# Kernel tuning notes

Measured on AMD Instinct MI355X. Metric: run time of the kernel, lower is better.

The kernel has to match this reference:

```python
import jax, jax.numpy as jnp
import numpy as np


def setup_inputs() -> dict:
    key = jax.random.key(0)
    ks = jax.random.split(key, 7)
    B, T, E, D = 4, 4096, 1024, 64
    s = 1.0 / np.sqrt(E)
    return {
        "x": jax.random.normal(ks[0], (B, T, E), dtype=jnp.float32),
        "Wq": jax.random.normal(ks[1], (E, D), dtype=jnp.float32) * s,
        "bq": jnp.zeros((D,), dtype=jnp.float32),
        "Wk": jax.random.normal(ks[2], (E, D), dtype=jnp.float32) * s,
        "bk": jnp.zeros((D,), dtype=jnp.float32),
        "Wv": jax.random.normal(ks[3], (E, D), dtype=jnp.float32) * s,
        "bv": jnp.zeros((D,), dtype=jnp.float32),
    }


def reference(x, Wq, bq, Wk, bk, Wv, bv):
    # Linear projections (torch Linear with W stored as [in, out])
    q = x @ Wq + bq  # [B, T, D]
    k = x @ Wk + bk  # [B, T, D]
    v = x @ Wv + bv  # [B, T, D]
    d_k = q.shape[-1]
    scale = 1.0 / jnp.sqrt(jnp.asarray(d_k, dtype=q.dtype))
    scores = jnp.einsum("btd,bsd->bts", q, k) * scale  # [B, T, T]
    att = jax.nn.softmax(scores, axis=-1)
    # dropout p=0.0 -> identity (eval-mode reference)
    out = jnp.einsum("bts,bsd->btd", att, v)  # [B, T, D]
    return out
```

## Files before the change

kernel.cpp:

```cpp
#include <hip/hip_runtime.h>

typedef __attribute__((ext_vector_type(4))) float f32x4;
typedef __attribute__((ext_vector_type(16))) float f32x16;
typedef __attribute__((ext_vector_type(8))) short s16x8;
typedef __attribute__((ext_vector_type(4))) short s16x4;
typedef __attribute__((ext_vector_type(4))) unsigned u32x4;

#define BATCH 4
#define SEQ 4096
#define EMB 1024
#define HD 64
#define QSCALE (0.125f * 1.44269504088896f)
#define M0 32.0f

static __device__ __forceinline__ unsigned short f2bf(float f) {
  union { float f; unsigned int u; } a;
  a.f = f;
  unsigned int u = a.u;
  u += 0x7FFFu + ((u >> 16) & 1u);
  return (unsigned short)(u >> 16);
}

static __device__ __forceinline__ float fexp2(float x) {
  return __builtin_amdgcn_exp2f(x);
}
static __device__ __forceinline__ void swap32u(unsigned& a, unsigned& b) {
  asm("s_nop 0\n\tv_permlane32_swap_b32 %0, %1\n\ts_nop 0" : "+v"(a), "+v"(b));
}
static __device__ __forceinline__ unsigned cvtpk(float lo, float hi) {
  unsigned r;
  asm("v_cvt_pk_bf16_f32 %0, %1, %2" : "=v"(r) : "v"(lo), "v"(hi));
  return r;
}

#define GLL16(g, l)                                                        \
  __builtin_amdgcn_global_load_lds(                                        \
      (const __attribute__((address_space(1))) unsigned int*)(g),          \
      (__attribute__((address_space(3))) unsigned int*)(l), 16, 0, 0)

__global__ __launch_bounds__(256) void k_wt(const float* __restrict__ Wq,
                                            const float* __restrict__ Wk,
                                            const float* __restrict__ Wv,
                                            unsigned short* __restrict__ wt) {
  __shared__ float lds[64][65];
  int tid = threadIdx.x;
  int which = blockIdx.x >> 4;
  int kt = blockIdx.x & 15;
  const float* W = (which == 0) ? Wq : ((which == 1) ? Wk : Wv);
#pragma unroll
  for (int i = 0; i < 4; ++i) {
    int idx = i * 256 + tid;
    int row = idx >> 4, c4 = idx & 15;
    float4 v = *(const float4*)(W + (size_t)(kt * 64 + row) * 64 + c4 * 4);
    lds[row][c4 * 4 + 0] = v.x;
    lds[row][c4 * 4 + 1] = v.y;
    lds[row][c4 * 4 + 2] = v.z;
    lds[row][c4 * 4 + 3] = v.w;
  }
  __syncthreads();
#pragma unroll
  for (int i = 0; i < 2; ++i) {
    int c = i * 256 + tid;
    int cfl = c >> 7, kk = (c >> 6) & 1, l = c & 63;
    int lg = l >> 4, lc = l & 15;
    s16x8 v;
#pragma unroll
    for (int j = 0; j < 8; ++j) v[j] = (short)f2bf(lds[kk * 32 + lg * 8 + j][cfl * 16 + lc]);
    size_t off = ((((size_t)kt * 12 + (which * 4 + cfl)) * 2 + kk) * 64 + l) * 8;
    *(s16x8*)(wt + off) = v;
  }
}

__global__ __launch_bounds__(256, 2) void k_proj(const float* __restrict__ x,
                                                 const unsigned short* __restrict__ wt,
                                                 const float* __restrict__ bq,
                                                 const float* __restrict__ bk,
                                                 const float* __restrict__ bv,
                                                 unsigned short* __restrict__ qws,
                                                 unsigned short* __restrict__ kws,
                                                 unsigned short* __restrict__ vws) {
  __shared__ char xb[4][8192];
  int tid = threadIdx.x;
  int w = tid >> 6, ln = tid & 63;
  int lg = ln >> 4, lc = ln & 15;
  int m0 = blockIdx.x * 32;

  f32x4 acc[2][3];
#pragma unroll
  for (int s = 0; s < 2; ++s)
#pragma unroll
    for (int c = 0; c < 3; ++c) acc[s][c] = (f32x4){0.f, 0.f, 0.f, 0.f};

  s16x8 bA[3][2], bB[3][2];

  int srow = w * 8 + (ln >> 4);
  int schunk0 = ln & 15;
#define GLLI(kt_, bi_)                                                        \
  _Pragma("unroll") for (int p = 0; p < 2; ++p) {                             \
    int r = srow + p * 4;                                                     \
    const char* src = (const char*)x + (size_t)(m0 + r) * 4096 + (kt_)*256 +  \
                      ((schunk0 ^ (r & 7)) << 4);                             \
    GLL16(src, &xb[bi_][w * 2048 + p * 1024]);                                \
  }
#define BLD(dst_, kt_)                                                        \
  _Pragma("unroll") for (int c = 0; c < 3; ++c)                               \
      _Pragma("unroll") for (int kk = 0; kk < 2; ++kk)                        \
          dst_[c][kk] = *(const s16x8*)(wt + ((size_t)((kt_)*12 + w * 3 + c) * 2 + kk) * 512 + ln * 8);

#define ITER(T_, bcur_, bnext_, NW_)                                          \
  {                                                                           \
    if ((T_) + 1 < 16) BLD(bnext_, (T_) + 1);                                 \
    if ((T_) + 3 < 16) GLLI((T_) + 3, ((T_) + 3) & 3);                        \
    asm volatile("s_waitcnt vmcnt(" #NW_ ")" ::: "memory");                   \
    __builtin_amdgcn_s_barrier();                                             \
    __builtin_amdgcn_sched_barrier(0);                                        \
    s16x8 a[2][2];                                                            \
    _Pragma("unroll") for (int s = 0; s < 2; ++s)                             \
        _Pragma("unroll") for (int kk = 0; kk < 2; ++kk) {                    \
      int g0 = kk * 8 + lg * 2;                                               \
      f32x4 c0 = *(const f32x4*)(&xb[(T_) & 3][(s * 16 + lc) * 256 + ((g0 ^ (lc & 7)) << 4)]); \
      f32x4 c1 = *(const f32x4*)(&xb[(T_) & 3][(s * 16 + lc) * 256 + (((g0 + 1) ^ (lc & 7)) << 4)]); \
      union { u32x4 u; s16x8 v; } cv;                                         \
      cv.u = (u32x4){cvtpk(c0[0], c0[1]), cvtpk(c0[2], c0[3]),                \
                     cvtpk(c1[0], c1[1]), cvtpk(c1[2], c1[3])};               \
      a[s][kk] = cv.v;                                                        \
    }                                                                         \
    __builtin_amdgcn_s_setprio(1);                                            \
    _Pragma("unroll") for (int s = 0; s < 2; ++s)                             \
        _Pragma("unroll") for (int c = 0; c < 3; ++c)                         \
            _Pragma("unroll") for (int kk = 0; kk < 2; ++kk)                  \
                acc[s][c] = __builtin_amdgcn_mfma_f32_16x16x32_bf16(          \
                    a[s][kk], bcur_[c][kk], acc[s][c], 0, 0, 0);              \
    __builtin_amdgcn_s_setprio(0);                                            \
    __builtin_amdgcn_s_barrier();                                             \
  }

  GLLI(0, 0);
  GLLI(1, 1);
  GLLI(2, 2);
  BLD(bA, 0);
  ITER(0, bA, bB, 18)
  ITER(1, bB, bA, 24)
  ITER(2, bA, bB, 30)
  ITER(3, bB, bA, 24)
  ITER(4, bA, bB, 24)
  ITER(5, bB, bA, 24)
  ITER(6, bA, bB, 24)
  ITER(7, bB, bA, 24)
  ITER(8, bA, bB, 24)
  ITER(9, bB, bA, 24)
  ITER(10, bA, bB, 24)
  ITER(11, bB, bA, 24)
  ITER(12, bA, bB, 24)
  ITER(13, bB, bA, 22)
  ITER(14, bA, bB, 20)
  ITER(15, bB, bA, 12)
#undef GLLI
#undef BLD
#undef ITER

  unsigned short* ep = (unsigned short*)&xb[0][0];
#pragma unroll
  for (int c = 0; c < 3; ++c) {
    int cf = w * 3 + c;
    int which = cf >> 2;
    int ncol = (cf & 3) * 16 + lc;
    float bias = (which == 0) ? bq[ncol] : ((which == 1) ? bk[ncol] : bv[ncol]);
    if (which < 2) {
#pragma unroll
      for (int s = 0; s < 2; ++s)
#pragma unroll
        for (int r = 0; r < 4; ++r) {
          int trow = s * 16 + lg * 4 + r;
          float val = acc[s][c][r] + bias;
          if (which == 0) val *= QSCALE;
          int o = (ncol >> 4) * 512 + ((ncol >> 3) & 1) * 256 + trow * 8 + (ncol & 7);
          ep[which * 2048 + o] = f2bf(val);
        }
    } else {
#pragma unroll
      for (int s = 0; s < 2; ++s) {
        s16x4 pk;
#pragma unroll
        for (int r = 0; r < 4; ++r) pk[r] = (short)f2bf(acc[s][c][r] + bias);
        int o = s * 1024 + (ncol >> 5) * 512 + (lg >> 1) * 256 + (ncol & 31) * 8 + (lg & 1) * 4;
        *(s16x4*)(ep + 2 * 2048 + o) = pk;
      }
    }
  }
  __syncthreads();
  {
    int b = m0 >> 12, tt = m0 & 4095;
    unsigned short* qdst = qws + (size_t)b * SEQ * 64 + (tt >> 5) * 2048;
    unsigned short* kdst = kws + (size_t)b * SEQ * 64 + (tt >> 5) * 2048;
    unsigned short* vdst = vws + (size_t)b * SEQ * 64 + (tt >> 4) * 1024;
#pragma unroll
    for (int k = 0; k < 3; ++k) {
      int u = k * 256 + tid;
      s16x8 val = *(const s16x8*)(ep + u * 8);
      int which = u >> 8;
      int o = (u & 255) * 8;
      unsigned short* dst = (which == 0) ? qdst : ((which == 1) ? kdst : vdst);
      *(s16x8*)(dst + o) = val;
    }
  }
}

template <int NS, int REP>
__global__ __launch_bounds__(256, 3) void k_attn(const unsigned short* __restrict__ qf_g,
                                                 const unsigned short* __restrict__ kf_g,
                                                 const unsigned short* __restrict__ vf_g,
                                                 float* __restrict__ part,
                                                 float2* __restrict__ ml) {
  __shared__ char kv[3][16384];
  int tid = threadIdx.x;
  int w = tid >> 6, ln = tid & 63;
  int F = blockIdx.x;
  const int nb = 128 * NS;
  int idx = (F & 7) * (nb >> 3) + (F >> 3);
  int split = idx >> 7;
  int rem = idx & 127;
  int b = rem >> 5, q7 = rem & 31;
  const int TPS = 64 / NS;
  int t0 = split * TPS;

  const unsigned short* qb = qf_g + (size_t)b * SEQ * 64;
  const char* kbytes = (const char*)(kf_g + (size_t)b * SEQ * 64);
  const char* vbytes = (const char*)(vf_g + (size_t)b * SEQ * 64);

  int qrow = q7 * 128 + w * 32;

  s16x8 qf[4];
#pragma unroll
  for (int db = 0; db < 4; ++db)
    qf[db] = *(const s16x8*)(qb + (size_t)(((q7 * 4 + w) * 4 + db) * 512 + ln * 8));

  s16x8 onef;
#pragma unroll
  for (int j = 0; j < 8; ++j) onef[j] = (short)0x3F80;

  f32x16 o_[2], l_acc;

#define STAGE(t_, bi_)                                                        \
  _Pragma("unroll") for (int i = 0; i < 4; ++i) {                             \
    int cc = w * 4 + i;                                                       \
    const char* src = (cc < 8 ? kbytes + (size_t)(t_)*8192 + cc * 1024        \
                              : vbytes + (size_t)(t_)*8192 + (cc - 8) * 1024) \
                      + ln * 16;                                              \
    GLL16(src, &kv[bi_][cc * 1024]);                                          \
  }

#pragma unroll 1
  for (int rep = 0; rep < REP; ++rep) {
#pragma unroll
    for (int dt = 0; dt < 2; ++dt)
#pragma unroll
      for (int i = 0; i < 16; ++i) o_[dt][i] = 0.f;
#pragma unroll
    for (int i = 0; i < 16; ++i) l_acc[i] = 0.f;

    STAGE(t0, 0)
    STAGE(t0 + 1, 1)
    int bi = 0;
#pragma unroll 1
    for (int it = 0; it < TPS; ++it) {
      int t = t0 + it;
      if (it + 2 < TPS) {
        int nbuf = (bi == 0) ? 2 : bi - 1;
        STAGE(t + 2, nbuf)
        asm volatile("s_waitcnt vmcnt(8)" ::: "memory");
      } else if (it + 1 < TPS) {
        asm volatile("s_waitcnt vmcnt(4)" ::: "memory");
      } else {
        asm volatile("s_waitcnt vmcnt(0)" ::: "memory");
      }
      __builtin_amdgcn_s_barrier();
      __builtin_amdgcn_sched_barrier(0);

      s16x8 kfc[2][4];
#pragma unroll
      for (int kt = 0; kt < 2; ++kt)
#pragma unroll
        for (int db = 0; db < 4; ++db)
          kfc[kt][db] = *(const s16x8*)(&kv[bi][(kt * 4 + db) * 1024 + ln * 16]);

      f32x16 s[2];
      __builtin_amdgcn_s_setprio(1);
#pragma unroll
      for (int kt = 0; kt < 2; ++kt) {
        f32x16 a;
#pragma unroll
        for (int i = 0; i < 16; ++i) a[i] = -M0;
#pragma unroll
        for (int db = 0; db < 4; ++db)
          a = __builtin_amdgcn_mfma_f32_32x32x16_bf16(kfc[kt][db], qf[db], a, 0, 0, 0);
        s[kt] = a;
      }
      __builtin_amdgcn_s_setprio(0);

      s16x8 pf[4];
      {
#pragma unroll
        for (int kt = 0; kt < 2; ++kt)
#pragma unroll
          for (int i = 0; i < 16; ++i) s[kt][i] = fexp2(s[kt][i]);
#pragma unroll
        for (int k4 = 0; k4 < 4; ++k4) {
          int kt = k4 >> 1, mr = 2 * (k4 & 1);
          unsigned a0 = cvtpk(s[kt][mr * 4 + 0], s[kt][mr * 4 + 1]);
          unsigned a1 = cvtpk(s[kt][mr * 4 + 2], s[kt][mr * 4 + 3]);
          unsigned b0 = cvtpk(s[kt][mr * 4 + 4], s[kt][mr * 4 + 5]);
          unsigned b1 = cvtpk(s[kt][mr * 4 + 6], s[kt][mr * 4 + 7]);
          swap32u(a0, b0);
          swap32u(a1, b1);
          union { u32x4 u; s16x8 v16; } cvt;
          cvt.u = (u32x4){a0, a1, b0, b1};
          pf[k4] = cvt.v16;
        }
      }

      __builtin_amdgcn_s_setprio(1);
#pragma unroll
      for (int dt = 0; dt < 2; ++dt)
#pragma unroll
        for (int k4 = 0; k4 < 4; ++k4) {
          s16x8 vfr = *(const s16x8*)(&kv[bi][8192 + (k4 * 2 + dt) * 1024 + ln * 16]);
          o_[dt] = __builtin_amdgcn_mfma_f32_32x32x16_bf16(vfr, pf[k4], o_[dt], 0, 0, 0);
        }
#pragma unroll
      for (int k4 = 0; k4 < 4; ++k4)
        l_acc = __builtin_amdgcn_mfma_f32_32x32x16_bf16(onef, pf[k4], l_acc, 0, 0, 0);
      __builtin_amdgcn_s_setprio(0);
      __builtin_amdgcn_s_barrier();
      bi = (bi == 2) ? 0 : bi + 1;
    }
    if (REP > 1) asm volatile("" : "+v"(o_[0]), "+v"(o_[1]), "+v"(l_acc));
  }
#undef STAGE

  float* pb = part + (size_t)(split * 4 + b) * 64 * SEQ;
  int hi = ln >> 5, lq = ln & 31;
  int tq = qrow + lq;
#pragma unroll
  for (int dt = 0; dt < 2; ++dt)
#pragma unroll
    for (int re = 0; re < 16; ++re) {
      int d = dt * 32 + (re & 3) + 8 * (re >> 2) + 4 * hi;
      pb[(size_t)d * SEQ + tq] = o_[dt][re];
    }
  if (ln < 32)
    ml[(size_t)(split * 4 + b) * SEQ + qrow + ln] = make_float2(M0, l_acc[0]);
}

template <int NS>
__global__ __launch_bounds__(256) void k_red(const float* __restrict__ part,
                                             const float2* __restrict__ ml,
                                             float* __restrict__ out) {
  __shared__ float lds[16][65];
  int tid = threadIdx.x;
  int w = tid >> 6, ln = tid & 63;
  int dq = blockIdx.x & 3;
  int t0 = (blockIdx.x >> 2) * 64;
  int b = t0 >> 12;
  int tt = (t0 & 4095) + ln;

  float2 mls[NS];
#pragma unroll
  for (int s = 0; s < NS; ++s) mls[s] = ml[(size_t)(s * 4 + b) * SEQ + tt];
  float M = mls[0].x;
#pragma unroll
  for (int s = 1; s < NS; ++s) M = fmaxf(M, mls[s].x);
  float Lden = 0.f;
#pragma unroll
  for (int s = 0; s < NS; ++s) Lden += mls[s].y * fexp2(mls[s].x - M);
  float inv = 1.0f / Lden;
  float sc[NS];
#pragma unroll
  for (int s = 0; s < NS; ++s) sc[s] = fexp2(mls[s].x - M) * inv;

  float acc[4] = {0.f, 0.f, 0.f, 0.f};
#pragma unroll
  for (int s = 0; s < NS; ++s) {
    const float* pb = part + ((size_t)(s * 4 + b) * 64 + dq * 16 + w * 4) * SEQ + tt;
#pragma unroll
    for (int i = 0; i < 4; ++i) acc[i] += sc[s] * pb[(size_t)i * SEQ];
  }
#pragma unroll
  for (int i = 0; i < 4; ++i) lds[w * 4 + i][ln] = acc[i];
  __syncthreads();
  {
    int tr = tid >> 2, dc = tid & 3;
    f32x4 o;
#pragma unroll
    for (int j = 0; j < 4; ++j) o[j] = lds[dc * 4 + j][tr];
    *(f32x4*)(out + (size_t)(t0 + tr) * 64 + dq * 16 + dc * 4) = o;
  }
}

extern "C" void kernel_launch(void* const* d_in, const int* in_sizes, int n_in,
                              void* d_out, int out_size, void* d_ws, size_t ws_size,
                              hipStream_t stream) {
  const float* x = (const float*)d_in[0];
  const float* Wq = (const float*)d_in[1];
  const float* bq = (const float*)d_in[2];
  const float* Wk = (const float*)d_in[3];
  const float* bk = (const float*)d_in[4];
  const float* Wv = (const float*)d_in[5];
  const float* bv = (const float*)d_in[6];
  float* out = (float*)d_out;

  char* ws = (char*)d_ws;
  unsigned short* wt = (unsigned short*)(ws);
  unsigned short* qws = (unsigned short*)(ws + 0x80000);
  unsigned short* kws = (unsigned short*)(ws + 0x280000);
  unsigned short* vws = (unsigned short*)(ws + 0x480000);
  const size_t base = 0x680000;
  const size_t perSplit = (size_t)16384 * 64 * 4 + (size_t)16384 * 8;

  k_wt<<<48, 256, 0, stream>>>(Wq, Wk, Wv, wt);
  k_proj<<<512, 256, 0, stream>>>(x, wt, bq, bk, bv, qws, kws, vws);

#define RUN_NS(NSV)                                                           \
  {                                                                           \
    float* partp = (float*)(ws + base);                                       \
    float2* mlp = (float2*)(ws + base + (size_t)NSV * 16384 * 64 * 4);        \
    k_attn<NSV, 1><<<128 * NSV, 256, 0, stream>>>(qws, kws, vws, partp, mlp); \
    k_red<NSV><<<1024, 256, 0, stream>>>(partp, mlp, out);                    \
  }

  if (ws_size >= base + 8 * perSplit) {
    RUN_NS(8)
  } else if (ws_size >= base + 4 * perSplit) {
    RUN_NS(4)
  } else if (ws_size >= base + 2 * perSplit) {
    RUN_NS(2)
  } else {
    RUN_NS(1)
  }
#undef RUN_NS
}
```

Before: 61.60 us.

## Halve KV tile to 32 keys, use 4-buffer ring and drop trailing barrier

Each pipeline stage now loads 32 keys instead of 64, so a stage holds 8 KB of K/V, and the ring grows to four buffers. With four buffers and a prefetch distance of two, the end-of-iteration barrier can go, leaving one barrier per step. Less LDS per block and a higher launch_bounds occupancy hint (5) allow more resident blocks. The cost is twice as many iterations, each with a barrier, waitcnt and a shorter MFMA chain, so there is less work per sync point.

```diff
diff --git a/kernel.cpp b/kernel.cpp
--- a/kernel.cpp
+++ b/kernel.cpp
@@ -207,12 +207,12 @@
 }
 
 template <int NS, int REP>
-__global__ __launch_bounds__(256, 3) void k_attn(const unsigned short* __restrict__ qf_g,
+__global__ __launch_bounds__(256, 5) void k_attn(const unsigned short* __restrict__ qf_g,
                                                  const unsigned short* __restrict__ kf_g,
                                                  const unsigned short* __restrict__ vf_g,
                                                  float* __restrict__ part,
                                                  float2* __restrict__ ml) {
-  __shared__ char kv[3][16384];
+  __shared__ char kv[4][8192];
   int tid = threadIdx.x;
   int w = tid >> 6, ln = tid & 63;
   int F = blockIdx.x;
@@ -221,8 +221,8 @@
   int split = idx >> 7;
   int rem = idx & 127;
   int b = rem >> 5, q7 = rem & 31;
-  const int TPS = 64 / NS;
-  int t0 = split * TPS;
+  const int TPS = 128 / NS;
+  int g0 = split * TPS;
 
   const unsigned short* qb = qf_g + (size_t)b * SEQ * 64;
   const char* kbytes = (const char*)(kf_g + (size_t)b * SEQ * 64);
@@ -241,11 +241,11 @@
 
   f32x16 o_[2], l_acc;
 
-#define STAGE(t_, bi_)                                                        \
-  _Pragma("unroll") for (int i = 0; i < 4; ++i) {                             \
-    int cc = w * 4 + i;                                                       \
-    const char* src = (cc < 8 ? kbytes + (size_t)(t_)*8192 + cc * 1024        \
-                              : vbytes + (size_t)(t_)*8192 + (cc - 8) * 1024) \
+#define STAGE(g_, bi_)                                                        \
+  _Pragma("unroll") for (int i = 0; i < 2; ++i) {                             \
+    int cc = w * 2 + i;                                                       \
+    const char* src = (cc < 4 ? kbytes + (size_t)(g_)*4096 + cc * 1024        \
+                              : vbytes + (size_t)(g_)*4096 + (cc - 4) * 1024) \
                       + ln * 16;                                              \
     GLL16(src, &kv[bi_][cc * 1024]);                                          \
   }
@@ -259,58 +259,52 @@
 #pragma unroll
     for (int i = 0; i < 16; ++i) l_acc[i] = 0.f;
 
-    STAGE(t0, 0)
-    STAGE(t0 + 1, 1)
-    int bi = 0;
+    STAGE(g0, 0)
+    STAGE(g0 + 1, 1)
 #pragma unroll 1
     for (int it = 0; it < TPS; ++it) {
-      int t = t0 + it;
+      int g = g0 + it;
+      int bi = it & 3;
       if (it + 2 < TPS) {
-        int nbuf = (bi == 0) ? 2 : bi - 1;
-        STAGE(t + 2, nbuf)
-        asm volatile("s_waitcnt vmcnt(8)" ::: "memory");
+        STAGE(g + 2, (it + 2) & 3)
+        asm volatile("s_waitcnt vmcnt(4)" ::: "memory");
       } else if (it + 1 < TPS) {
-        asm volatile("s_waitcnt vmcnt(4)" ::: "memory");
+        asm volatile("s_waitcnt vmcnt(2)" ::: "memory");
       } else {
         asm volatile("s_waitcnt vmcnt(0)" ::: "memory");
       }
       __builtin_amdgcn_s_barrier();
       __builtin_amdgcn_sched_barrier(0);
 
-      s16x8 kfc[2][4];
-#pragma unroll
-      for (int kt = 0; kt < 2; ++kt)
+      s16x8 kfc[4];
+#pragma unroll
+      for (int db = 0; db < 4; ++db)
+        kfc[db] = *(const s16x8*)(&kv[bi][db * 1024 + ln * 16]);
+
+      f32x16 s;
+      __builtin_amdgcn_s_setprio(1);
+      {
+        f32x16 a;
+#pragma unroll
+        for (int i = 0; i < 16; ++i) a[i] = -M0;
 #pragma unroll
         for (int db = 0; db < 4; ++db)
-          kfc[kt][db] = *(const s16x8*)(&kv[bi][(kt * 4 + db) * 1024 + ln * 16]);
-
-      f32x16 s[2];
-      __builtin_amdgcn_s_setprio(1);
-#pragma unroll
-      for (int kt = 0; kt < 2; ++kt) {
-        f32x16 a;
-#pragma unroll
-        for (int i = 0; i < 16; ++i) a[i] = -M0;
-#pragma unroll
-        for (int db = 0; db < 4; ++db)
-          a = __builtin_amdgcn_mfma_f32_32x32x16_bf16(kfc[kt][db], qf[db], a, 0, 0, 0);
-        s[kt] = a;
+          a = __builtin_amdgcn_mfma_f32_32x32x16_bf16(kfc[db], qf[db], a, 0, 0, 0);
+        s = a;
       }
       __builtin_amdgcn_s_setprio(0);
 
-      s16x8 pf[4];
+      s16x8 pf[2];
       {
 #pragma unroll
-        for (int kt = 0; kt < 2; ++kt)
-#pragma unroll
-          for (int i = 0; i < 16; ++i) s[kt][i] = fexp2(s[kt][i]);
-#pragma unroll
-        for (int k4 = 0; k4 < 4; ++k4) {
-          int kt = k4 >> 1, mr = 2 * (k4 & 1);
-          unsigned a0 = cvtpk(s[kt][mr * 4 + 0], s[kt][mr * 4 + 1]);
-          unsigned a1 = cvtpk(s[kt][mr * 4 + 2], s[kt][mr * 4 + 3]);
-          unsigned b0 = cvtpk(s[kt][mr * 4 + 4], s[kt][mr * 4 + 5]);
-          unsigned b1 = cvtpk(s[kt][mr * 4 + 6], s[kt][mr * 4 + 7]);
+        for (int i = 0; i < 16; ++i) s[i] = fexp2(s[i]);
+#pragma unroll
+        for (int k4 = 0; k4 < 2; ++k4) {
+          int mr = 2 * k4;
+          unsigned a0 = cvtpk(s[mr * 4 + 0], s[mr * 4 + 1]);
+          unsigned a1 = cvtpk(s[mr * 4 + 2], s[mr * 4 + 3]);
+          unsigned b0 = cvtpk(s[mr * 4 + 4], s[mr * 4 + 5]);
+          unsigned b1 = cvtpk(s[mr * 4 + 6], s[mr * 4 + 7]);
           swap32u(a0, b0);
           swap32u(a1, b1);
           union { u32x4 u; s16x8 v16; } cvt;
@@ -323,16 +317,14 @@
 #pragma unroll
       for (int dt = 0; dt < 2; ++dt)
 #pragma unroll
-        for (int k4 = 0; k4 < 4; ++k4) {
-          s16x8 vfr = *(const s16x8*)(&kv[bi][8192 + (k4 * 2 + dt) * 1024 + ln * 16]);
+        for (int k4 = 0; k4 < 2; ++k4) {
+          s16x8 vfr = *(const s16x8*)(&kv[bi][4096 + (k4 * 2 + dt) * 1024 + ln * 16]);
           o_[dt] = __builtin_amdgcn_mfma_f32_32x32x16_bf16(vfr, pf[k4], o_[dt], 0, 0, 0);
         }
 #pragma unroll
-      for (int k4 = 0; k4 < 4; ++k4)
+      for (int k4 = 0; k4 < 2; ++k4)
         l_acc = __builtin_amdgcn_mfma_f32_32x32x16_bf16(onef, pf[k4], l_acc, 0, 0, 0);
       __builtin_amdgcn_s_setprio(0);
-      __builtin_amdgcn_s_barrier();
-      bi = (bi == 2) ? 0 : bi + 1;
     }
     if (REP > 1) asm volatile("" : "+v"(o_[0]), "+v"(o_[1]), "+v"(l_acc));
   }
```

Result: slower. 75.27 us (+22.2%).
